# Kernel optimization log

Measured on AMD Instinct MI355X. Metric: run time of the kernel, lower is better.

The kernel has to match this reference:

```python
import jax, jax.numpy as jnp
import numpy as np

H = 1024        # hidden_size
E = 8           # num_experts
K = 2           # top_k
FF = 4 * H      # expert hidden dim
B, S = 2, 2048


def setup_inputs() -> dict:
    key = jax.random.key(0)
    ks = jax.random.split(key, 7)
    scale = 0.02
    x = jax.random.normal(ks[0], (B, S, H), dtype=jnp.float32)
    Wg = jax.random.normal(ks[1], (H, E), dtype=jnp.float32) * scale
    bg = jnp.zeros((E,), dtype=jnp.float32)
    W1 = jax.random.normal(ks[2], (E, H, FF), dtype=jnp.float32) * scale
    b1 = jnp.zeros((E, FF), dtype=jnp.float32)
    W2 = jax.random.normal(ks[3], (E, FF, H), dtype=jnp.float32) * scale
    b2 = jnp.zeros((E, H), dtype=jnp.float32)
    return {"x": x, "Wg": Wg, "bg": bg, "W1": W1, "b1": b1, "W2": W2, "b2": b2}


def reference(x, Wg, bg, W1, b1, W2, b2):
    b, s, h = x.shape
    xf = x.reshape(-1, h)                                  # [T, H]
    T = xf.shape[0]
    # gating: softmax -> top-k -> renormalize
    probs = jax.nn.softmax(xf @ Wg + bg, axis=-1)          # [T, E]
    vals, idx = jax.lax.top_k(probs, K)                    # [T, K]
    vals = vals / jnp.sum(vals, axis=-1, keepdims=True)
    # dense combine weights: zero for non-selected experts (equivalent math)
    combine = jnp.zeros((T, E), dtype=x.dtype)
    combine = combine.at[jnp.arange(T)[:, None], idx].set(vals)  # [T, E]
    # all-expert FFN (GEMM-dominated), combined with sparse gate weights
    hmid = jax.nn.gelu(jnp.einsum('th,ehf->tef', xf, W1) + b1, approximate=False)  # [T,E,FF]
    y = jnp.einsum('tef,efh->teh', hmid, W2) + b2          # [T, E, H]
    out = jnp.einsum('te,teh->th', combine, y)             # [T, H]
    return out.reshape(b, s, h)
```

## Files before the change

kernel.cpp:

```cpp
#include <hip/hip_runtime.h>
#include <hip/hip_bf16.h>
#include <math.h>

#define T_TOK  4096
#define H_DIM  1024
#define E_NUM  8
#define FF_DIM 4096
#define KSEL   2
#define SLOTS  (T_TOK*KSEL)
#define SLOTS_PAD (SLOTS + 128)
#define BM 128
#define MAXTILES 72

typedef __attribute__((ext_vector_type(8))) short s16x8;
typedef __attribute__((ext_vector_type(8))) unsigned short u16x8;
typedef __attribute__((ext_vector_type(4))) float f32x4;

typedef __attribute__((address_space(1))) const void global_cvoid;
typedef __attribute__((address_space(3))) void lds_void;

__device__ __forceinline__ unsigned short f2bf(float f){
  unsigned int u = __float_as_uint(f);
  u += 0x7fffu + ((u>>16)&1u);
  return (unsigned short)(u>>16);
}
__device__ __forceinline__ float bf2f(unsigned short h){
  return __uint_as_float(((unsigned int)h)<<16);
}

static constexpr size_t OFF_CNT   = 0;
static constexpr size_t OFF_OFFS  = 256;
static constexpr size_t OFF_NT    = 512;
static constexpr size_t OFF_TILES = 768;
static constexpr size_t OFF_IDX   = 1280;
static constexpr size_t OFF_POS   = OFF_IDX  + 32768;
static constexpr size_t OFF_WV    = OFF_POS  + 32768;
static constexpr size_t OFF_SLOT  = OFF_WV   + 32768;
static constexpr size_t OFF_TOK   = OFF_SLOT + 32768;
static constexpr size_t OFF_WOF   = OFF_TOK  + 32768;
static constexpr size_t OFF_XG    = OFF_WOF  + 32768;
static constexpr size_t OFF_W1T   = OFF_XG  + (size_t)SLOTS_PAD*H_DIM*2;
static constexpr size_t OFF_W2T   = OFF_W1T + (size_t)E_NUM*H_DIM*FF_DIM*2;
static constexpr size_t OFF_MID   = OFF_W2T + (size_t)E_NUM*H_DIM*FF_DIM*2;
static constexpr size_t OFF_Y     = OFF_MID + (size_t)SLOTS_PAD*FF_DIM*2;

__global__ __launch_bounds__(64) void gate_kernel(
    const float* __restrict__ x, const float* __restrict__ Wg,
    const float* __restrict__ bg, int* __restrict__ cnt,
    int* __restrict__ idxp, int* __restrict__ posp, float* __restrict__ wvp)
{
  int t = blockIdx.x, lane = threadIdx.x;
  const float* xr = x + (size_t)t*H_DIM;
  float acc[E_NUM];
  #pragma unroll
  for (int e=0;e<E_NUM;e++) acc[e]=0.f;
  for (int i=0;i<H_DIM/64;i++){
    int h = i*64 + lane;
    float xv = xr[h];
    const float* wr_ = Wg + (size_t)h*E_NUM;
    #pragma unroll
    for (int e=0;e<E_NUM;e++) acc[e] += xv*wr_[e];
  }
  #pragma unroll
  for (int e=0;e<E_NUM;e++){
    #pragma unroll
    for (int off=32; off>0; off>>=1) acc[e] += __shfl_xor(acc[e], off);
  }
  if (lane==0){
    float l[E_NUM];
    #pragma unroll
    for (int e=0;e<E_NUM;e++) l[e] = acc[e] + bg[e];
    int i0 = 0;
    #pragma unroll
    for (int e=1;e<E_NUM;e++) if (l[e] > l[i0]) i0 = e;
    int i1 = (i0==0)?1:0;
    #pragma unroll
    for (int e=0;e<E_NUM;e++) if (e!=i0 && l[e] > l[i1]) i1 = e;
    float p1 = expf(l[i1]-l[i0]);
    float s  = 1.f + p1;
    float w0 = 1.f/s, w1 = p1/s;
    int pos0 = atomicAdd(&cnt[i0],1);
    int pos1 = atomicAdd(&cnt[i1],1);
    idxp[t*2]=i0; idxp[t*2+1]=i1;
    posp[t*2]=pos0; posp[t*2+1]=pos1;
    wvp[t*2]=w0; wvp[t*2+1]=w1;
  }
}

__global__ void plan_kernel(const int* __restrict__ cnt, int* __restrict__ offs,
                            int* __restrict__ tiles, int* __restrict__ ntiles)
{
  int o=0, n=0;
  for (int e=0;e<E_NUM;e++){
    offs[e]=o;
    int c=cnt[e];
    int nt=(c+BM-1)/BM;
    for (int m=0;m<nt;m++) tiles[n++] = (e<<16)|m;
    o+=c;
  }
  offs[E_NUM]=o;
  *ntiles=n;
}

__global__ void scatter_kernel(const int* __restrict__ idxp, const int* __restrict__ posp,
                               const float* __restrict__ wvp, const int* __restrict__ offs,
                               int* __restrict__ tok_of, float* __restrict__ w_of,
                               int* __restrict__ slot_of)
{
  int i = blockIdx.x*blockDim.x + threadIdx.x;
  if (i >= SLOTS) return;
  int t = i>>1, k = i&1;
  int e = idxp[t*2+k];
  int slot = offs[e] + posp[t*2+k];
  tok_of[slot] = t;
  w_of[slot]   = wvp[t*2+k];
  slot_of[t*2+k] = slot;
}

__global__ __launch_bounds__(256) void gather_kernel(
    const float* __restrict__ x, const int* __restrict__ tok_of,
    unsigned short* __restrict__ Xg)
{
  int slot = blockIdx.x;
  int t = tok_of[slot];
  const float4* src = (const float4*)(x + (size_t)t*H_DIM);
  float4 v = src[threadIdx.x];
  ushort4 o;
  o.x=f2bf(v.x); o.y=f2bf(v.y); o.z=f2bf(v.z); o.w=f2bf(v.w);
  ((ushort4*)(Xg + (size_t)slot*H_DIM))[threadIdx.x] = o;
}

__global__ __launch_bounds__(256) void transconv_kernel(
    const float* __restrict__ in, unsigned short* __restrict__ out, int R, int C)
{
  __shared__ float tile[64][65];
  int e = blockIdx.z;
  const float* inp = in + (size_t)e*R*C;
  unsigned short* op = out + (size_t)e*R*C;
  int c0 = blockIdx.x*64, r0 = blockIdx.y*64;
  int tx = threadIdx.x & 15, ty = threadIdx.x >> 4;
  #pragma unroll
  for (int i=0;i<4;i++){
    int r = i*16 + ty;
    float4 v = *(const float4*)(inp + (size_t)(r0+r)*C + c0 + tx*4);
    tile[r][tx*4+0]=v.x; tile[r][tx*4+1]=v.y; tile[r][tx*4+2]=v.z; tile[r][tx*4+3]=v.w;
  }
  __syncthreads();
  int wx = threadIdx.x & 7;
  int wcl = threadIdx.x >> 3;
  #pragma unroll
  for (int i=0;i<2;i++){
    int c = i*32 + wcl;
    u16x8 o;
    #pragma unroll
    for (int j=0;j<8;j++) o[j] = f2bf(tile[wx*8+j][c]);
    *(u16x8*)(op + (size_t)(c0+c)*R + r0 + wx*8) = o;
  }
}

template<int MODE>
__global__ __launch_bounds__(256) void gemm_kernel(
    const unsigned short* __restrict__ A,
    const unsigned short* __restrict__ Bt,
    const float* __restrict__ bias,
    unsigned short* __restrict__ Out,
    const int* __restrict__ tiles, const int* __restrict__ ntiles,
    const int* __restrict__ cnt, const int* __restrict__ offs,
    const float* __restrict__ w_of,
    int N, int K, int ncb_shift)
{
  int tile_id = blockIdx.x >> ncb_shift;
  if (tile_id >= *ntiles) return;
  int col0 = (blockIdx.x & ((1<<ncb_shift)-1)) << 7;
  int packed = tiles[tile_id];
  int e = packed>>16, mt = packed & 0xffff;
  int row0 = offs[e] + mt*BM;
  int nvalid = cnt[e] - mt*BM; if (nvalid > BM) nvalid = BM;
  const unsigned short* Be = Bt + (size_t)e*N*K;

  __shared__ unsigned short As[2][128*32];
  __shared__ unsigned short Bs[2][128*32];

  int t = threadIdx.x;
  int wid = t>>6, lane = t&63;
  int wr = (wid>>1)*64, wc = (wid&1)*64;
  int fr = lane&15, fq = lane>>4;
  int cb = wid*64;

  int c0c = cb + lane;
  int c1c = cb + 256 + lane;
  const unsigned short* gA0 = A  + (size_t)(row0 + (c0c>>2))*K + (c0c&3)*8;
  const unsigned short* gA1 = A  + (size_t)(row0 + (c1c>>2))*K + (c1c&3)*8;
  const unsigned short* gB0 = Be + (size_t)(col0 + (c0c>>2))*K + (c0c&3)*8;
  const unsigned short* gB1 = Be + (size_t)(col0 + (c1c>>2))*K + (c1c&3)*8;
  int ldsOff0 = cb*16, ldsOff1 = (cb+256)*16;

  auto stage = [&](int buf, int k0){
    __builtin_amdgcn_global_load_lds((global_cvoid*)(gA0 + k0),
        (lds_void*)((char*)&As[buf][0] + ldsOff0), 16, 0, 0);
    __builtin_amdgcn_global_load_lds((global_cvoid*)(gB0 + k0),
        (lds_void*)((char*)&Bs[buf][0] + ldsOff0), 16, 0, 0);
    __builtin_amdgcn_global_load_lds((global_cvoid*)(gA1 + k0),
        (lds_void*)((char*)&As[buf][0] + ldsOff1), 16, 0, 0);
    __builtin_amdgcn_global_load_lds((global_cvoid*)(gB1 + k0),
        (lds_void*)((char*)&Bs[buf][0] + ldsOff1), 16, 0, 0);
  };

  f32x4 acc[4][4];
  #pragma unroll
  for (int i=0;i<4;i++)
    #pragma unroll
    for (int j=0;j<4;j++) acc[i][j] = (f32x4){0.f,0.f,0.f,0.f};

  int NT = K >> 5;
  stage(0, 0);
  stage(1, 32);
  int cur = 0;
  for (int kt=0; kt<NT; ++kt){
    if (kt + 2 < NT) asm volatile("s_waitcnt vmcnt(4)" ::: "memory");
    else             asm volatile("s_waitcnt vmcnt(0)" ::: "memory");
    __builtin_amdgcn_s_barrier();

    s16x8 af[4], bfr[4];
    #pragma unroll
    for (int i=0;i<4;i++){
      af[i]  = *(const s16x8*)&As[cur][(wr + i*16 + fr)*32 + fq*8];
      bfr[i] = *(const s16x8*)&Bs[cur][(wc + i*16 + fr)*32 + fq*8];
    }
    #pragma unroll
    for (int i=0;i<4;i++)
      #pragma unroll
      for (int j=0;j<4;j++)
        acc[i][j] = __builtin_amdgcn_mfma_f32_16x16x32_bf16(af[i], bfr[j], acc[i][j], 0,0,0);

    asm volatile("s_waitcnt lgkmcnt(0)" ::: "memory");
    __builtin_amdgcn_s_barrier();
    if (kt + 2 < NT) stage(cur, (kt+2)*32);
    cur ^= 1;
  }

  #pragma unroll
  for (int i=0;i<4;i++){
    #pragma unroll
    for (int r=0;r<4;r++){
      int lrow = wr + i*16 + fq*4 + r;
      if (lrow < nvalid){
        int grow = row0 + lrow;
        float scale = (MODE==1) ? w_of[grow] : 0.f;
        #pragma unroll
        for (int j=0;j<4;j++){
          int col = col0 + wc + j*16 + fr;
          float v = acc[i][j][r] + bias[(size_t)e*N + col];
          if (MODE==0) v = 0.5f*v*(1.f + erff(v*0.70710678118654752f));
          else         v *= scale;
          Out[(size_t)grow*N + col] = f2bf(v);
        }
      }
    }
  }
}

__global__ __launch_bounds__(256) void combine_kernel(
    const unsigned short* __restrict__ y, const int* __restrict__ slot_of,
    float* __restrict__ out)
{
  int tok = blockIdx.x;
  int s0 = slot_of[tok*2], s1 = slot_of[tok*2+1];
  const ushort4* y0 = (const ushort4*)(y + (size_t)s0*H_DIM);
  const ushort4* y1 = (const ushort4*)(y + (size_t)s1*H_DIM);
  float4* o = (float4*)(out + (size_t)tok*H_DIM);
  ushort4 a = y0[threadIdx.x], b = y1[threadIdx.x];
  float4 r;
  r.x = bf2f(a.x)+bf2f(b.x);
  r.y = bf2f(a.y)+bf2f(b.y);
  r.z = bf2f(a.z)+bf2f(b.z);
  r.w = bf2f(a.w)+bf2f(b.w);
  o[threadIdx.x] = r;
}

extern "C" void kernel_launch(void* const* d_in, const int* in_sizes, int n_in,
                              void* d_out, int out_size, void* d_ws, size_t ws_size,
                              hipStream_t stream) {
  const float* x  = (const float*)d_in[0];
  const float* Wg = (const float*)d_in[1];
  const float* bg = (const float*)d_in[2];
  const float* W1 = (const float*)d_in[3];
  const float* b1 = (const float*)d_in[4];
  const float* W2 = (const float*)d_in[5];
  const float* b2 = (const float*)d_in[6];
  float* out = (float*)d_out;
  char* ws = (char*)d_ws;

  int*   cnt     = (int*)  (ws + OFF_CNT);
  int*   offs    = (int*)  (ws + OFF_OFFS);
  int*   ntiles  = (int*)  (ws + OFF_NT);
  int*   tiles   = (int*)  (ws + OFF_TILES);
  int*   idxp    = (int*)  (ws + OFF_IDX);
  int*   posp    = (int*)  (ws + OFF_POS);
  float* wvp     = (float*)(ws + OFF_WV);
  int*   slot_of = (int*)  (ws + OFF_SLOT);
  int*   tok_of  = (int*)  (ws + OFF_TOK);
  float* w_of    = (float*)(ws + OFF_WOF);
  unsigned short* Xg  = (unsigned short*)(ws + OFF_XG);
  unsigned short* W1t = (unsigned short*)(ws + OFF_W1T);
  unsigned short* W2t = (unsigned short*)(ws + OFF_W2T);
  unsigned short* mid = (unsigned short*)(ws + OFF_MID);
  unsigned short* y   = (unsigned short*)(ws + OFF_Y);

  hipMemsetAsync(ws + OFF_CNT, 0, 32, stream);

  gate_kernel<<<T_TOK, 64, 0, stream>>>(x, Wg, bg, cnt, idxp, posp, wvp);
  plan_kernel<<<1, 1, 0, stream>>>(cnt, offs, tiles, ntiles);
  scatter_kernel<<<SLOTS/256, 256, 0, stream>>>(idxp, posp, wvp, offs, tok_of, w_of, slot_of);
  gather_kernel<<<SLOTS, 256, 0, stream>>>(x, tok_of, Xg);

  transconv_kernel<<<dim3(FF_DIM/64, H_DIM/64, E_NUM), 256, 0, stream>>>(W1, W1t, H_DIM, FF_DIM);
  transconv_kernel<<<dim3(H_DIM/64, FF_DIM/64, E_NUM), 256, 0, stream>>>(W2, W2t, FF_DIM, H_DIM);

  gemm_kernel<0><<<dim3(MAXTILES*32), 256, 0, stream>>>(
      Xg, W1t, b1, mid, tiles, ntiles, cnt, offs, nullptr, FF_DIM, H_DIM, 5);
  gemm_kernel<1><<<dim3(MAXTILES*8), 256, 0, stream>>>(
      mid, W2t, b2, y, tiles, ntiles, cnt, offs, w_of, H_DIM, FF_DIM, 3);

  combine_kernel<<<T_TOK, 256, 0, stream>>>(y, slot_of, out);
}
```

Before: 470.9 us.

## Add 256x256 swizzled GEMM for first expert layer, triple-buffer second GEMM

Replaces the first expert GEMM (X·W1 with GELU) with a new 512-thread kernel using 256x256 output tiles, a 64-wide K step, XOR-swizzled LDS layout, and staged prefetch interleaved with MFMA groups and priority hints. The plan kernel now also emits a 256-row tile list. The second GEMM moves from double to triple buffering with deeper vmcnt waits and setprio around its MFMAs. The aim is more data reuse per tile and better overlap of loads with compute, at the cost of 128 KB LDS per block, possible register pressure, and more padding waste on partial 256-row tiles.

```diff
diff --git a/kernel.cpp b/kernel.cpp
--- a/kernel.cpp
+++ b/kernel.cpp
@@ -8,9 +8,10 @@
 #define FF_DIM 4096
 #define KSEL   2
 #define SLOTS  (T_TOK*KSEL)
-#define SLOTS_PAD (SLOTS + 128)
+#define SLOTS_PAD (SLOTS + 256)
 #define BM 128
 #define MAXTILES 72
+#define MAXT256  40
 
 typedef __attribute__((ext_vector_type(8))) short s16x8;
 typedef __attribute__((ext_vector_type(8))) unsigned short u16x8;
@@ -31,7 +32,9 @@
 static constexpr size_t OFF_CNT   = 0;
 static constexpr size_t OFF_OFFS  = 256;
 static constexpr size_t OFF_NT    = 512;
+static constexpr size_t OFF_NT256 = 516;
 static constexpr size_t OFF_TILES = 768;
+static constexpr size_t OFF_T256  = 1088;
 static constexpr size_t OFF_IDX   = 1280;
 static constexpr size_t OFF_POS   = OFF_IDX  + 32768;
 static constexpr size_t OFF_WV    = OFF_POS  + 32768;
@@ -88,18 +91,22 @@
 }
 
 __global__ void plan_kernel(const int* __restrict__ cnt, int* __restrict__ offs,
-                            int* __restrict__ tiles, int* __restrict__ ntiles)
-{
-  int o=0, n=0;
+                            int* __restrict__ tiles, int* __restrict__ ntiles,
+                            int* __restrict__ tiles256, int* __restrict__ ntiles256)
+{
+  int o=0, n=0, n2=0;
   for (int e=0;e<E_NUM;e++){
     offs[e]=o;
     int c=cnt[e];
     int nt=(c+BM-1)/BM;
     for (int m=0;m<nt;m++) tiles[n++] = (e<<16)|m;
+    int nt2=(c+255)/256;
+    for (int m=0;m<nt2;m++) tiles256[n2++] = (e<<16)|m;
     o+=c;
   }
   offs[E_NUM]=o;
   *ntiles=n;
+  *ntiles256=n2;
 }
 
 __global__ void scatter_kernel(const int* __restrict__ idxp, const int* __restrict__ posp,
@@ -158,7 +165,153 @@
   }
 }
 
-template<int MODE>
+#define GLDS(g, l) __builtin_amdgcn_global_load_lds((global_cvoid*)(g), (lds_void*)(l), 16, 0, 0)
+
+__global__ __launch_bounds__(512, 2) void gemm256_kernel(
+    const unsigned short* __restrict__ A,
+    const unsigned short* __restrict__ Bt,
+    const float* __restrict__ bias,
+    unsigned short* __restrict__ Out,
+    const int* __restrict__ tiles256, const int* __restrict__ ntiles256,
+    const int* __restrict__ cnt, const int* __restrict__ offs)
+{
+  constexpr int K = H_DIM, N = FF_DIM;
+  int tile_id = blockIdx.x >> 4;
+  if (tile_id >= *ntiles256) return;
+  int col0 = (blockIdx.x & 15) << 8;
+  int packed = tiles256[tile_id];
+  int e = packed>>16, mt = packed & 0xffff;
+  int row0 = offs[e] + mt*256;
+  int nvalid = cnt[e] - mt*256; if (nvalid > 256) nvalid = 256;
+  const unsigned short* Be = Bt + (size_t)e*N*K;
+
+  __shared__ unsigned short As[2][256*64];
+  __shared__ unsigned short Bs[2][256*64];
+
+  int t = threadIdx.x;
+  int wid = t>>6, lane = t&63;
+  int wm = wid>>2, wn = wid&3;
+  int fr = lane&15, fq = lane>>4;
+
+  int rl  = t>>3;
+  int ccl = (t&7) ^ (rl&7);
+  char* asb = (char*)&As[0][0];
+  char* bsb = (char*)&Bs[0][0];
+  int ldst = wid*1024;
+
+  #define STAGE_B(buf,j,kt) GLDS(Be + (size_t)(col0 + (j)*64 + rl)*K + (kt)*64 + ccl*8, \
+                                 bsb + (buf)*32768 + (j)*8192 + ldst)
+  #define STAGE_A(buf,j,kt) GLDS(A  + (size_t)(row0 + (j)*64 + rl)*K + (kt)*64 + ccl*8, \
+                                 asb + (buf)*32768 + (j)*8192 + ldst)
+  #define STAGEG(buf,g,kt) do{ \
+    if ((g)==0){ STAGE_B(buf,0,kt); STAGE_B(buf,1,kt); } \
+    else if ((g)==1){ STAGE_B(buf,2,kt); STAGE_B(buf,3,kt); } \
+    else if ((g)==2){ STAGE_A(buf,0,kt); STAGE_A(buf,2,kt); } \
+    else { STAGE_A(buf,1,kt); STAGE_A(buf,3,kt); } }while(0)
+
+  #define RD_A(buf,m,ks) (*(const s16x8*)(asb + (buf)*32768 + (wm*128+(m)*16+fr)*128 + ((((ks)*4+fq) ^ (fr&7))<<4)))
+  #define RD_B(buf,n,ks) (*(const s16x8*)(bsb + (buf)*32768 + (wn*64 +(n)*16+fr)*128 + ((((ks)*4+fq) ^ (fr&7))<<4)))
+
+  f32x4 acc[8][4];
+  #pragma unroll
+  for (int i=0;i<8;i++)
+    #pragma unroll
+    for (int j=0;j<4;j++) acc[i][j] = (f32x4){0.f,0.f,0.f,0.f};
+
+  s16x8 bfr[4][2];
+
+  constexpr int NT = K >> 6;
+  STAGEG(0,0,0); STAGEG(0,1,0); STAGEG(0,2,0); STAGEG(0,3,0);
+  asm volatile("s_waitcnt vmcnt(2)" ::: "memory");
+  __builtin_amdgcn_s_barrier();
+
+  #define MFMA_PAIR(m0, a00,a01,a10,a11) \
+    _Pragma("unroll") \
+    for (int n=0;n<4;n++){ \
+      acc[m0][n]   = __builtin_amdgcn_mfma_f32_16x16x32_bf16(a00, bfr[n][0], acc[m0][n],   0,0,0); \
+      acc[m0][n]   = __builtin_amdgcn_mfma_f32_16x16x32_bf16(a01, bfr[n][1], acc[m0][n],   0,0,0); \
+      acc[m0+1][n] = __builtin_amdgcn_mfma_f32_16x16x32_bf16(a10, bfr[n][0], acc[m0+1][n], 0,0,0); \
+      acc[m0+1][n] = __builtin_amdgcn_mfma_f32_16x16x32_bf16(a11, bfr[n][1], acc[m0+1][n], 0,0,0); \
+    }
+
+  for (int kt=0; kt<NT; ++kt){
+    int cur = kt&1, nxt = cur^1;
+    bool pf = (kt+1 < NT);
+    {
+      #pragma unroll
+      for (int n=0;n<4;n++){ bfr[n][0] = RD_B(cur,n,0); bfr[n][1] = RD_B(cur,n,1); }
+      s16x8 a00=RD_A(cur,0,0), a01=RD_A(cur,0,1), a10=RD_A(cur,1,0), a11=RD_A(cur,1,1);
+      if (pf) STAGEG(nxt,0,kt+1);
+      asm volatile("s_waitcnt lgkmcnt(0)" ::: "memory");
+      __builtin_amdgcn_sched_barrier(0);
+      __builtin_amdgcn_s_setprio(1);
+      MFMA_PAIR(0, a00,a01,a10,a11);
+      __builtin_amdgcn_s_setprio(0);
+      __builtin_amdgcn_s_barrier();
+    }
+    {
+      s16x8 a00=RD_A(cur,2,0), a01=RD_A(cur,2,1), a10=RD_A(cur,3,0), a11=RD_A(cur,3,1);
+      if (pf) STAGEG(nxt,1,kt+1);
+      asm volatile("s_waitcnt lgkmcnt(0)" ::: "memory");
+      __builtin_amdgcn_sched_barrier(0);
+      __builtin_amdgcn_s_setprio(1);
+      MFMA_PAIR(2, a00,a01,a10,a11);
+      __builtin_amdgcn_s_setprio(0);
+      if (pf) asm volatile("s_waitcnt vmcnt(4)" ::: "memory");
+      else    asm volatile("s_waitcnt vmcnt(0)" ::: "memory");
+      __builtin_amdgcn_s_barrier();
+    }
+    {
+      s16x8 a00=RD_A(cur,4,0), a01=RD_A(cur,4,1), a10=RD_A(cur,5,0), a11=RD_A(cur,5,1);
+      if (pf) STAGEG(nxt,2,kt+1);
+      asm volatile("s_waitcnt lgkmcnt(0)" ::: "memory");
+      __builtin_amdgcn_sched_barrier(0);
+      __builtin_amdgcn_s_setprio(1);
+      MFMA_PAIR(4, a00,a01,a10,a11);
+      __builtin_amdgcn_s_setprio(0);
+      __builtin_amdgcn_s_barrier();
+    }
+    {
+      s16x8 a00=RD_A(cur,6,0), a01=RD_A(cur,6,1), a10=RD_A(cur,7,0), a11=RD_A(cur,7,1);
+      if (pf) STAGEG(nxt,3,kt+1);
+      asm volatile("s_waitcnt lgkmcnt(0)" ::: "memory");
+      __builtin_amdgcn_sched_barrier(0);
+      __builtin_amdgcn_s_setprio(1);
+      MFMA_PAIR(6, a00,a01,a10,a11);
+      __builtin_amdgcn_s_setprio(0);
+      asm volatile("s_waitcnt vmcnt(2)" ::: "memory");
+      __builtin_amdgcn_s_barrier();
+    }
+  }
+
+  float bias_v[4];
+  #pragma unroll
+  for (int n=0;n<4;n++) bias_v[n] = bias[(size_t)e*N + col0 + wn*64 + n*16 + fr];
+  #pragma unroll
+  for (int m=0;m<8;m++){
+    #pragma unroll
+    for (int r=0;r<4;r++){
+      int lrow = wm*128 + m*16 + fq*4 + r;
+      if (lrow < nvalid){
+        int grow = row0 + lrow;
+        #pragma unroll
+        for (int n=0;n<4;n++){
+          int col = col0 + wn*64 + n*16 + fr;
+          float v = acc[m][n][r] + bias_v[n];
+          v = 0.5f*v*(1.f + erff(v*0.70710678118654752f));
+          Out[(size_t)grow*N + col] = f2bf(v);
+        }
+      }
+    }
+  }
+  #undef STAGE_B
+  #undef STAGE_A
+  #undef STAGEG
+  #undef RD_A
+  #undef RD_B
+  #undef MFMA_PAIR
+}
+
 __global__ __launch_bounds__(256) void gemm_kernel(
     const unsigned short* __restrict__ A,
     const unsigned short* __restrict__ Bt,
@@ -178,8 +331,8 @@
   int nvalid = cnt[e] - mt*BM; if (nvalid > BM) nvalid = BM;
   const unsigned short* Be = Bt + (size_t)e*N*K;
 
-  __shared__ unsigned short As[2][128*32];
-  __shared__ unsigned short Bs[2][128*32];
+  __shared__ unsigned short As[3][128*32];
+  __shared__ unsigned short Bs[3][128*32];
 
   int t = threadIdx.x;
   int wid = t>>6, lane = t&63;
@@ -196,14 +349,10 @@
   int ldsOff0 = cb*16, ldsOff1 = (cb+256)*16;
 
   auto stage = [&](int buf, int k0){
-    __builtin_amdgcn_global_load_lds((global_cvoid*)(gA0 + k0),
-        (lds_void*)((char*)&As[buf][0] + ldsOff0), 16, 0, 0);
-    __builtin_amdgcn_global_load_lds((global_cvoid*)(gB0 + k0),
-        (lds_void*)((char*)&Bs[buf][0] + ldsOff0), 16, 0, 0);
-    __builtin_amdgcn_global_load_lds((global_cvoid*)(gA1 + k0),
-        (lds_void*)((char*)&As[buf][0] + ldsOff1), 16, 0, 0);
-    __builtin_amdgcn_global_load_lds((global_cvoid*)(gB1 + k0),
-        (lds_void*)((char*)&Bs[buf][0] + ldsOff1), 16, 0, 0);
+    GLDS(gA0 + k0, (char*)&As[buf][0] + ldsOff0);
+    GLDS(gB0 + k0, (char*)&Bs[buf][0] + ldsOff0);
+    GLDS(gA1 + k0, (char*)&As[buf][0] + ldsOff1);
+    GLDS(gB1 + k0, (char*)&Bs[buf][0] + ldsOff1);
   };
 
   f32x4 acc[4][4];
@@ -213,12 +362,13 @@
     for (int j=0;j<4;j++) acc[i][j] = (f32x4){0.f,0.f,0.f,0.f};
 
   int NT = K >> 5;
-  stage(0, 0);
-  stage(1, 32);
-  int cur = 0;
+  stage(0, 0); stage(1, 32); stage(2, 64);
   for (int kt=0; kt<NT; ++kt){
-    if (kt + 2 < NT) asm volatile("s_waitcnt vmcnt(4)" ::: "memory");
-    else             asm volatile("s_waitcnt vmcnt(0)" ::: "memory");
+    int cur = kt - (kt/3)*3;
+    int ahead = NT-1-kt;
+    if (ahead>=2)      asm volatile("s_waitcnt vmcnt(8)" ::: "memory");
+    else if (ahead==1) asm volatile("s_waitcnt vmcnt(4)" ::: "memory");
+    else               asm volatile("s_waitcnt vmcnt(0)" ::: "memory");
     __builtin_amdgcn_s_barrier();
 
     s16x8 af[4], bfr[4];
@@ -227,16 +377,20 @@
       af[i]  = *(const s16x8*)&As[cur][(wr + i*16 + fr)*32 + fq*8];
       bfr[i] = *(const s16x8*)&Bs[cur][(wc + i*16 + fr)*32 + fq*8];
     }
+    __builtin_amdgcn_s_setprio(1);
     #pragma unroll
     for (int i=0;i<4;i++)
       #pragma unroll
       for (int j=0;j<4;j++)
         acc[i][j] = __builtin_amdgcn_mfma_f32_16x16x32_bf16(af[i], bfr[j], acc[i][j], 0,0,0);
+    __builtin_amdgcn_s_setprio(0);
 
     asm volatile("s_waitcnt lgkmcnt(0)" ::: "memory");
     __builtin_amdgcn_s_barrier();
-    if (kt + 2 < NT) stage(cur, (kt+2)*32);
-    cur ^= 1;
+    if (kt + 3 < NT){
+      int nb = kt+3; nb = nb - (nb/3)*3;
+      stage(nb, (kt+3)*32);
+    }
   }
 
   #pragma unroll
@@ -246,13 +400,12 @@
       int lrow = wr + i*16 + fq*4 + r;
       if (lrow < nvalid){
         int grow = row0 + lrow;
-        float scale = (MODE==1) ? w_of[grow] : 0.f;
+        float scale = w_of[grow];
         #pragma unroll
         for (int j=0;j<4;j++){
           int col = col0 + wc + j*16 + fr;
           float v = acc[i][j][r] + bias[(size_t)e*N + col];
-          if (MODE==0) v = 0.5f*v*(1.f + erff(v*0.70710678118654752f));
-          else         v *= scale;
+          v *= scale;
           Out[(size_t)grow*N + col] = f2bf(v);
         }
       }
@@ -291,16 +444,18 @@
   float* out = (float*)d_out;
   char* ws = (char*)d_ws;
 
-  int*   cnt     = (int*)  (ws + OFF_CNT);
-  int*   offs    = (int*)  (ws + OFF_OFFS);
-  int*   ntiles  = (int*)  (ws + OFF_NT);
-  int*   tiles   = (int*)  (ws + OFF_TILES);
-  int*   idxp    = (int*)  (ws + OFF_IDX);
-  int*   posp    = (int*)  (ws + OFF_POS);
-  float* wvp     = (float*)(ws + OFF_WV);
-  int*   slot_of = (int*)  (ws + OFF_SLOT);
-  int*   tok_of  = (int*)  (ws + OFF_TOK);
-  float* w_of    = (float*)(ws + OFF_WOF);
+  int*   cnt      = (int*)  (ws + OFF_CNT);
+  int*   offs     = (int*)  (ws + OFF_OFFS);
+  int*   ntiles   = (int*)  (ws + OFF_NT);
+  int*   ntiles256= (int*)  (ws + OFF_NT256);
+  int*   tiles    = (int*)  (ws + OFF_TILES);
+  int*   tiles256 = (int*)  (ws + OFF_T256);
+  int*   idxp     = (int*)  (ws + OFF_IDX);
+  int*   posp     = (int*)  (ws + OFF_POS);
+  float* wvp      = (float*)(ws + OFF_WV);
+  int*   slot_of  = (int*)  (ws + OFF_SLOT);
+  int*   tok_of   = (int*)  (ws + OFF_TOK);
+  float* w_of     = (float*)(ws + OFF_WOF);
   unsigned short* Xg  = (unsigned short*)(ws + OFF_XG);
   unsigned short* W1t = (unsigned short*)(ws + OFF_W1T);
   unsigned short* W2t = (unsigned short*)(ws + OFF_W2T);
@@ -310,16 +465,16 @@
   hipMemsetAsync(ws + OFF_CNT, 0, 32, stream);
 
   gate_kernel<<<T_TOK, 64, 0, stream>>>(x, Wg, bg, cnt, idxp, posp, wvp);
-  plan_kernel<<<1, 1, 0, stream>>>(cnt, offs, tiles, ntiles);
+  plan_kernel<<<1, 1, 0, stream>>>(cnt, offs, tiles, ntiles, tiles256, ntiles256);
   scatter_kernel<<<SLOTS/256, 256, 0, stream>>>(idxp, posp, wvp, offs, tok_of, w_of, slot_of);
   gather_kernel<<<SLOTS, 256, 0, stream>>>(x, tok_of, Xg);
 
   transconv_kernel<<<dim3(FF_DIM/64, H_DIM/64, E_NUM), 256, 0, stream>>>(W1, W1t, H_DIM, FF_DIM);
   transconv_kernel<<<dim3(H_DIM/64, FF_DIM/64, E_NUM), 256, 0, stream>>>(W2, W2t, FF_DIM, H_DIM);
 
-  gemm_kernel<0><<<dim3(MAXTILES*32), 256, 0, stream>>>(
-      Xg, W1t, b1, mid, tiles, ntiles, cnt, offs, nullptr, FF_DIM, H_DIM, 5);
-  gemm_kernel<1><<<dim3(MAXTILES*8), 256, 0, stream>>>(
+  gemm256_kernel<<<dim3(MAXT256*16), 512, 0, stream>>>(
+      Xg, W1t, b1, mid, tiles256, ntiles256, cnt, offs);
+  gemm_kernel<<<dim3(MAXTILES*8), 256, 0, stream>>>(
       mid, W2t, b2, y, tiles, ntiles, cnt, offs, w_of, H_DIM, FF_DIM, 3);
 
   combine_kernel<<<T_TOK, 256, 0, stream>>>(y, slot_of, out);
```

New measurement: 485.8 us. 1.03x slower.
